# Optimization experiments

Hardware: AMD Instinct MI355X
Metric: run time of the kernel (lower is better)

## Reference

```python
import jax, jax.numpy as jnp
import numpy as np

NUM_GRAPHS = 256


def _mean_aggregate(h, src, dst, num_nodes):
    # DGL copy_src + mean reduce: dst node gets mean of src-node features over in-edges.
    summed = jax.ops.segment_sum(h[src], dst, num_segments=num_nodes)  # [N, F]
    deg = jax.ops.segment_sum(jnp.ones((src.shape[0],), h.dtype), dst, num_segments=num_nodes)
    return summed / jnp.maximum(deg, 1.0)[:, None]


def setup_inputs() -> dict:
    key = jax.random.key(0)
    ks = jax.random.split(key, 10)
    N, E, D_IN, H1, H2, OUT = 50000, 800000, 128, 256, 128, 1
    s = lambda fan: 1.0 / np.sqrt(fan)
    return {
        "h": jax.random.normal(ks[0], (N, D_IN), jnp.float32),
        "src": jax.random.randint(ks[1], (E,), 0, N),
        "dst": jax.random.randint(ks[2], (E,), 0, N),
        "graph_ids": jnp.sort(jax.random.randint(ks[3], (N,), 0, NUM_GRAPHS)),
        "W1": jax.random.normal(ks[4], (D_IN, H1), jnp.float32) * s(D_IN),
        "b1": jnp.zeros((H1,), jnp.float32),
        "W2": jax.random.normal(ks[5], (H1, H1), jnp.float32) * s(H1),
        "b2": jnp.zeros((H1,), jnp.float32),
        "Wr1": jax.random.normal(ks[6], (H1, H2), jnp.float32) * s(H1),
        "br1": jnp.zeros((H2,), jnp.float32),
        "Wr2": jax.random.normal(ks[7], (H2, OUT), jnp.float32) * s(H2),
        "br2": jnp.zeros((OUT,), jnp.float32),
    }


def reference(h, src, dst, graph_ids, W1, b1, W2, b2, Wr1, br1, Wr2, br2):
    N = h.shape[0]
    # GCN layer 1: mean-aggregate then linear+ReLU
    h = _mean_aggregate(h, src, dst, N)
    h = jax.nn.relu(h @ W1 + b1)
    # GCN layer 2
    h = _mean_aggregate(h, src, dst, N)
    h = jax.nn.relu(h @ W2 + b2)
    # dgl.mean_nodes readout: per-graph mean of node features
    gsum = jax.ops.segment_sum(h, graph_ids, num_segments=NUM_GRAPHS)  # [G, H1]
    gcnt = jax.ops.segment_sum(jnp.ones((N,), h.dtype), graph_ids, num_segments=NUM_GRAPHS)
    hg = gsum / jnp.maximum(gcnt, 1.0)[:, None]
    hidden = hg @ Wr1 + br1
    return hidden @ Wr2 + br2  # [G, 1]
```

## Files before the change

### kernel.cpp

```cpp
#include <hip/hip_runtime.h>


#define NUM_GRAPHS 256

#define CNT_B0 0
#define CNT_NB 1024
#define CST_B0 (CNT_B0 + CNT_NB)
#define CST_NB 512
#define GST_B0 (CST_B0 + CST_NB)
#define GST_NB 64
#define WT1_B0 (GST_B0 + GST_NB)
#define WT1_NB 16
#define WT2_B0 (WT1_B0 + WT1_NB)
#define WT2_NB 32
#define MISC_NB (WT2_B0 + WT2_NB)

typedef __attribute__((ext_vector_type(8))) short bf16x8;
typedef __attribute__((ext_vector_type(4))) float f32x4;

__device__ inline unsigned short f2bf(float f) {
    unsigned u = __float_as_uint(f);
    return (unsigned short)((u + 0x7fff + ((u >> 16) & 1)) >> 16);
}
__device__ inline float bflo(unsigned u) { return __uint_as_float(u << 16); }
__device__ inline float bfhi(unsigned u) { return __uint_as_float(u & 0xffff0000u); }


__launch_bounds__(256)
__global__ void misc_kernel(const int* __restrict__ dst, const int* __restrict__ gids,
                            const float* __restrict__ h,
                            const float* __restrict__ W1, const float* __restrict__ W2,
                            int* __restrict__ cnt, int* __restrict__ gstart,
                            unsigned short* __restrict__ hb,
                            unsigned short* __restrict__ Wt1, unsigned short* __restrict__ Wt2,
                            int N, int E) {
    int b = blockIdx.x, tid = threadIdx.x;
    if (b < CST_B0) {
        int lid = (b - CNT_B0) * 256 + tid;
        for (int e = lid; e < E; e += CNT_NB * 256) atomicAdd(&cnt[dst[e]], 1);
    } else if (b < GST_B0) {
        int lid = (b - CST_B0) * 256 + tid;
        int total4 = N * 32;
        for (int i = lid; i < total4; i += CST_NB * 256) {
            float4 v = *(const float4*)(h + (size_t)i * 4);
            ushort4 o;
            o.x = f2bf(v.x); o.y = f2bf(v.y); o.z = f2bf(v.z); o.w = f2bf(v.w);
            *(ushort4*)(hb + (size_t)i * 4) = o;
        }
    } else if (b < WT1_B0) {
        int lid = (b - GST_B0) * 256 + tid;
        for (int n = lid; n < N; n += GST_NB * 256) {
            int g = gids[n];
            int gp = (n == 0) ? -1 : gids[n - 1];
            for (int x = gp + 1; x <= g; ++x) gstart[x] = n;
            if (n == N - 1)
                for (int x = g + 1; x <= NUM_GRAPHS; ++x) gstart[x] = N;
        }
    } else if (b < WT2_B0) {
        int lid = (b - WT1_B0) * 256 + tid;
        for (int i = lid; i < 256 * 128; i += WT1_NB * 256)
            Wt1[i] = f2bf(W1[(size_t)(i & 127) * 256 + (i >> 7)]);
    } else {
        int lid = (b - WT2_B0) * 256 + tid;
        for (int i = lid; i < 256 * 256; i += WT2_NB * 256)
            Wt2[i] = f2bf(W2[(size_t)(i & 255) * 256 + (i >> 8)]);
    }
}


__global__ void scan1_kernel(const int* __restrict__ cnt, int* __restrict__ offs,
                             int* __restrict__ part, int N) {
    __shared__ int wsum[16];
    int tid = threadIdx.x;
    int lane = tid & 63;
    int wid = tid >> 6;
    int i = blockIdx.x * 1024 + tid;
    int v = (i < N) ? cnt[i] : 0;
    int x = v;
    #pragma unroll
    for (int d = 1; d < 64; d <<= 1) {
        int y = __shfl_up(x, d, 64);
        if (lane >= d) x += y;
    }
    if (lane == 63) wsum[wid] = x;
    __syncthreads();
    if (wid == 0) {
        int s = (lane < 16) ? wsum[lane] : 0;
        #pragma unroll
        for (int d = 1; d < 16; d <<= 1) {
            int y = __shfl_up(s, d, 64);
            if (lane >= d) s += y;
        }
        if (lane < 16) wsum[lane] = s;
    }
    __syncthreads();
    int wbase = (wid > 0) ? wsum[wid - 1] : 0;
    if (i < N) offs[i] = wbase + x - v;
    if (tid == 1023) part[blockIdx.x] = wbase + x;
}

__global__ void scan23_kernel(int* __restrict__ offs, const int* __restrict__ part,
                              int N, int E) {
    int b = blockIdx.x;
    int base = 0;
    for (int j = 0; j < b; ++j) base += part[j];
    int i = b * 1024 + threadIdx.x;
    if (i < N) offs[i] += base;
    if (b == 0 && threadIdx.x == 0) offs[N] = E;
}

__global__ void scatter_kernel(const int* __restrict__ src, const int* __restrict__ dst,
                               const int* __restrict__ offs, int* __restrict__ cnt,
                               int* __restrict__ eidx, int E) {
    int e = blockIdx.x * blockDim.x + threadIdx.x;
    if (e < E) {
        int d = dst[e];
        int p = offs[d] + atomicSub(&cnt[d], 1) - 1;
        eidx[p] = src[e];
    }
}


template <int D>
__global__ void agg_mean_bf16_kernel(const unsigned short* __restrict__ feat,
                                     const int* __restrict__ offs,
                                     const int* __restrict__ eidx,
                                     unsigned short* __restrict__ out, int N) {
    constexpr int VPL = D / 64;
    int wave = blockIdx.x * (blockDim.x >> 6) + (threadIdx.x >> 6);
    int lane = threadIdx.x & 63;
    if (wave >= N) return;
    int beg = offs[wave], end = offs[wave + 1];
    float acc[VPL];
    #pragma unroll
    for (int i = 0; i < VPL; ++i) acc[i] = 0.0f;

    int j = beg;
    for (; j + 8 <= end; j += 8) {
        int s[8];
        #pragma unroll
        for (int u = 0; u < 8; ++u) s[u] = eidx[j + u];
        if constexpr (VPL == 2) {
            unsigned v[8];
            #pragma unroll
            for (int u = 0; u < 8; ++u)
                v[u] = *(const unsigned*)(feat + (size_t)s[u] * D + lane * 2);
            #pragma unroll
            for (int u = 0; u < 8; ++u) { acc[0] += bflo(v[u]); acc[1] += bfhi(v[u]); }
        } else {
            uint2 v[8];
            #pragma unroll
            for (int u = 0; u < 8; ++u)
                v[u] = *(const uint2*)(feat + (size_t)s[u] * D + lane * 4);
            #pragma unroll
            for (int u = 0; u < 8; ++u) {
                acc[0] += bflo(v[u].x); acc[1] += bfhi(v[u].x);
                acc[2] += bflo(v[u].y); acc[3] += bfhi(v[u].y);
            }
        }
    }
    for (; j < end; ++j) {
        int s = eidx[j];
        if constexpr (VPL == 2) {
            unsigned v = *(const unsigned*)(feat + (size_t)s * D + lane * 2);
            acc[0] += bflo(v); acc[1] += bfhi(v);
        } else {
            uint2 v = *(const uint2*)(feat + (size_t)s * D + lane * 4);
            acc[0] += bflo(v.x); acc[1] += bfhi(v.x);
            acc[2] += bflo(v.y); acc[3] += bfhi(v.y);
        }
    }

    int deg = end - beg;
    float invd = 1.0f / (float)(deg > 0 ? deg : 1);
    unsigned short* orow = out + (size_t)wave * D + lane * VPL;
    if constexpr (VPL == 2) {
        ushort2 o; o.x = f2bf(acc[0] * invd); o.y = f2bf(acc[1] * invd);
        *(ushort2*)orow = o;
    } else {
        ushort4 o;
        o.x = f2bf(acc[0] * invd); o.y = f2bf(acc[1] * invd);
        o.z = f2bf(acc[2] * invd); o.w = f2bf(acc[3] * invd);
        *(ushort4*)orow = o;
    }
}


template <int K, int MODE>
__launch_bounds__(256)
__global__ void gemm_mfma_kernel(const unsigned short* __restrict__ A,
                                 const unsigned short* __restrict__ Wt,
                                 const float* __restrict__ bias,
                                 unsigned short* __restrict__ Cb,
                                 const int* __restrict__ gids,
                                 float* __restrict__ gsum,
                                 int N) {
    constexpr int LDS = 40;
    __shared__ unsigned short As[64 * LDS];
    __shared__ unsigned short Bs[256 * LDS];

    int tid = threadIdx.x;
    int wave = tid >> 6;
    int lane = tid & 63;
    int m = lane & 15;
    int q = lane >> 4;
    int rowBase = blockIdx.x * 64;

    f32x4 acc[4][4] = {};

    for (int kc = 0; kc < K; kc += 32) {
        {
            int r = tid >> 2;
            int seg = tid & 3;
            int gr = rowBase + r;
            uint4 v = make_uint4(0, 0, 0, 0);
            if (gr < N) v = *(const uint4*)(A + (size_t)gr * K + kc + seg * 8);
            *(uint4*)&As[r * LDS + seg * 8] = v;
        }
        #pragma unroll
        for (int it = 0; it < 4; ++it) {
            int n = (tid >> 2) + it * 64;
            int seg = tid & 3;
            uint4 v = *(const uint4*)(Wt + (size_t)n * K + kc + seg * 8);
            *(uint4*)&Bs[n * LDS + seg * 8] = v;
        }
        __syncthreads();

        bf16x8 af[4], bfr[4];
        #pragma unroll
        for (int r = 0; r < 4; ++r)
            af[r] = *(const bf16x8*)&As[(r * 16 + m) * LDS + q * 8];
        #pragma unroll
        for (int c = 0; c < 4; ++c)
            bfr[c] = *(const bf16x8*)&Bs[(wave * 64 + c * 16 + m) * LDS + q * 8];
        #pragma unroll
        for (int r = 0; r < 4; ++r)
            #pragma unroll
            for (int c = 0; c < 4; ++c)
                acc[r][c] = __builtin_amdgcn_mfma_f32_16x16x32_bf16(af[r], bfr[c], acc[r][c], 0, 0, 0);
        __syncthreads();
    }

    if constexpr (MODE == 0) {
        #pragma unroll
        for (int c = 0; c < 4; ++c) {
            int col = wave * 64 + c * 16 + m;
            float bv = bias[col];
            #pragma unroll
            for (int r = 0; r < 4; ++r) {
                #pragma unroll
                for (int reg = 0; reg < 4; ++reg) {
                    int grow = rowBase + r * 16 + q * 4 + reg;
                    if (grow < N)
                        Cb[(size_t)grow * 256 + col] = f2bf(fmaxf(acc[r][c][reg] + bv, 0.0f));
                }
            }
        }
    } else {
        int* sgid = (int*)As;
        if (tid < 64) {
            int gr = rowBase + tid;
            sgid[tid] = (gr < N) ? gids[gr] : -1;
        }
        __syncthreads();
        #pragma unroll
        for (int c = 0; c < 4; ++c) {
            int col = wave * 64 + c * 16 + m;
            float bv = bias[col];
            float partsum = 0.0f;
            int gprev = -1;
            #pragma unroll
            for (int r = 0; r < 4; ++r) {
                #pragma unroll
                for (int reg = 0; reg < 4; ++reg) {
                    int lr = r * 16 + q * 4 + reg;
                    if (rowBase + lr < N) {
                        int g = sgid[lr];
                        float o = fmaxf(acc[r][c][reg] + bv, 0.0f);
                        if (g != gprev) {
                            if (gprev >= 0) atomicAdd(&gsum[gprev * 256 + col], partsum);
                            partsum = 0.0f;
                            gprev = g;
                        }
                        partsum += o;
                    }
                }
            }
            if (gprev >= 0) atomicAdd(&gsum[gprev * 256 + col], partsum);
        }
    }
}


__global__ void final_kernel(const float* __restrict__ gsum, const int* __restrict__ gstart,
                             const float* __restrict__ Wr1, const float* __restrict__ br1,
                             const float* __restrict__ Wr2, const float* __restrict__ br2,
                             float* __restrict__ out) {
    int g = blockIdx.x;
    int j = threadIdx.x;
    int c = gstart[g + 1] - gstart[g];
    float invc = 1.0f / (float)(c > 0 ? c : 1);
    const float* gs = gsum + g * 256;
    float acc = br1[j];
    for (int k = 0; k < 256; ++k)
        acc += (gs[k] * invc) * Wr1[k * 128 + j];
    float p = acc * Wr2[j];
    #pragma unroll
    for (int d = 32; d > 0; d >>= 1) p += __shfl_down(p, d, 64);
    __shared__ float ws2[2];
    if ((j & 63) == 0) ws2[j >> 6] = p;
    __syncthreads();
    if (j == 0) out[g] = ws2[0] + ws2[1] + br2[0];
}


extern "C" void kernel_launch(void* const* d_in, const int* in_sizes, int n_in,
                              void* d_out, int out_size, void* d_ws, size_t ws_size,
                              hipStream_t stream) {
    const float* h    = (const float*)d_in[0];
    const int*   src  = (const int*)d_in[1];
    const int*   dst  = (const int*)d_in[2];
    const int*   gids = (const int*)d_in[3];
    const float* W1   = (const float*)d_in[4];
    const float* b1   = (const float*)d_in[5];
    const float* W2   = (const float*)d_in[6];
    const float* b2   = (const float*)d_in[7];
    const float* Wr1  = (const float*)d_in[8];
    const float* br1  = (const float*)d_in[9];
    const float* Wr2  = (const float*)d_in[10];
    const float* br2  = (const float*)d_in[11];

    int N = in_sizes[0] / 128;
    int E = in_sizes[1];
    int nScanBlocks = (N + 1023) / 1024;

    char* w = (char*)d_ws;
    unsigned short* hb     = (unsigned short*)w;  w += (size_t)N * 128 * sizeof(unsigned short);
    unsigned short* h1b    = (unsigned short*)w;  w += (size_t)N * 256 * sizeof(unsigned short);
    unsigned short* aggOut = (unsigned short*)w;  w += (size_t)N * 256 * sizeof(unsigned short);
    int* cnt    = (int*)w;              w += (size_t)N * sizeof(int);
    float* gsum = (float*)w;            w += (size_t)NUM_GRAPHS * 256 * sizeof(float);
    int* offs   = (int*)w;              w += (size_t)(N + 1) * sizeof(int);
    int* eidx   = (int*)w;              w += (size_t)E * sizeof(int);
    int* part   = (int*)w;              w += 64 * sizeof(int);
    unsigned short* Wt1 = (unsigned short*)w;  w += 256 * 128 * sizeof(unsigned short);
    unsigned short* Wt2 = (unsigned short*)w;  w += 256 * 256 * sizeof(unsigned short);
    int* gstart = (int*)w;              w += (size_t)(NUM_GRAPHS + 1) * sizeof(int);

    hipMemsetAsync(cnt, 0, (size_t)N * sizeof(int) + (size_t)NUM_GRAPHS * 256 * sizeof(float),
                   stream);
    misc_kernel<<<MISC_NB, 256, 0, stream>>>(dst, gids, h, W1, W2, cnt, gstart, hb, Wt1, Wt2, N, E);
    scan1_kernel<<<nScanBlocks, 1024, 0, stream>>>(cnt, offs, part, N);
    scan23_kernel<<<nScanBlocks, 1024, 0, stream>>>(offs, part, N, E);
    scatter_kernel<<<(E + 255) / 256, 256, 0, stream>>>(src, dst, offs, cnt, eidx, E);

    agg_mean_bf16_kernel<128><<<(N + 3) / 4, 256, 0, stream>>>(hb, offs, eidx, aggOut, N);
    gemm_mfma_kernel<128, 0><<<(N + 63) / 64, 256, 0, stream>>>(aggOut, Wt1, b1, h1b, nullptr, nullptr, N);

    agg_mean_bf16_kernel<256><<<(N + 3) / 4, 256, 0, stream>>>(h1b, offs, eidx, aggOut, N);
    gemm_mfma_kernel<256, 1><<<(N + 63) / 64, 256, 0, stream>>>(aggOut, Wt2, b2, nullptr, gids, gsum, N);

    final_kernel<<<NUM_GRAPHS, 128, 0, stream>>>(gsum, gstart, Wr1, br1, Wr2, br2, (float*)d_out);
}
```

Baseline: 346.9 us.

## Fuse mean aggregation into MFMA GEMM and precompute edge ranks for CSR scatter

```diff
diff --git a/kernel.cpp b/kernel.cpp
--- a/kernel.cpp
+++ b/kernel.cpp
@@ -30,14 +30,19 @@
 __global__ void misc_kernel(const int* __restrict__ dst, const int* __restrict__ gids,
                             const float* __restrict__ h,
                             const float* __restrict__ W1, const float* __restrict__ W2,
-                            int* __restrict__ cnt, int* __restrict__ gstart,
+                            int* __restrict__ cnt, int* __restrict__ rank,
+                            int* __restrict__ gstart,
                             unsigned short* __restrict__ hb,
                             unsigned short* __restrict__ Wt1, unsigned short* __restrict__ Wt2,
                             int N, int E) {
     int b = blockIdx.x, tid = threadIdx.x;
     if (b < CST_B0) {
         int lid = (b - CNT_B0) * 256 + tid;
-        for (int e = lid; e < E; e += CNT_NB * 256) atomicAdd(&cnt[dst[e]], 1);
+        for (int e = lid; e < E; e += CNT_NB * 256) {
+            int d = __builtin_nontemporal_load(&dst[e]);
+            int r = atomicAdd(&cnt[d], 1);
+            __builtin_nontemporal_store(r, &rank[e]);
+        }
     } else if (b < GST_B0) {
         int lid = (b - CST_B0) * 256 + tid;
         int total4 = N * 32;
@@ -109,132 +114,127 @@
     if (b == 0 && threadIdx.x == 0) offs[N] = E;
 }
 
+
 __global__ void scatter_kernel(const int* __restrict__ src, const int* __restrict__ dst,
-                               const int* __restrict__ offs, int* __restrict__ cnt,
+                               const int* __restrict__ offs, const int* __restrict__ rank,
                                int* __restrict__ eidx, int E) {
     int e = blockIdx.x * blockDim.x + threadIdx.x;
     if (e < E) {
-        int d = dst[e];
-        int p = offs[d] + atomicSub(&cnt[d], 1) - 1;
-        eidx[p] = src[e];
-    }
-}
-
-
-template <int D>
-__global__ void agg_mean_bf16_kernel(const unsigned short* __restrict__ feat,
-                                     const int* __restrict__ offs,
-                                     const int* __restrict__ eidx,
-                                     unsigned short* __restrict__ out, int N) {
-    constexpr int VPL = D / 64;
-    int wave = blockIdx.x * (blockDim.x >> 6) + (threadIdx.x >> 6);
-    int lane = threadIdx.x & 63;
-    if (wave >= N) return;
-    int beg = offs[wave], end = offs[wave + 1];
-    float acc[VPL];
-    #pragma unroll
-    for (int i = 0; i < VPL; ++i) acc[i] = 0.0f;
-
-    int j = beg;
-    for (; j + 8 <= end; j += 8) {
-        int s[8];
-        #pragma unroll
-        for (int u = 0; u < 8; ++u) s[u] = eidx[j + u];
-        if constexpr (VPL == 2) {
-            unsigned v[8];
-            #pragma unroll
-            for (int u = 0; u < 8; ++u)
-                v[u] = *(const unsigned*)(feat + (size_t)s[u] * D + lane * 2);
-            #pragma unroll
-            for (int u = 0; u < 8; ++u) { acc[0] += bflo(v[u]); acc[1] += bfhi(v[u]); }
-        } else {
-            uint2 v[8];
-            #pragma unroll
-            for (int u = 0; u < 8; ++u)
-                v[u] = *(const uint2*)(feat + (size_t)s[u] * D + lane * 4);
-            #pragma unroll
-            for (int u = 0; u < 8; ++u) {
-                acc[0] += bflo(v[u].x); acc[1] += bfhi(v[u].x);
-                acc[2] += bflo(v[u].y); acc[3] += bfhi(v[u].y);
-            }
-        }
-    }
-    for (; j < end; ++j) {
-        int s = eidx[j];
-        if constexpr (VPL == 2) {
-            unsigned v = *(const unsigned*)(feat + (size_t)s * D + lane * 2);
-            acc[0] += bflo(v); acc[1] += bfhi(v);
-        } else {
-            uint2 v = *(const uint2*)(feat + (size_t)s * D + lane * 4);
-            acc[0] += bflo(v.x); acc[1] += bfhi(v.x);
-            acc[2] += bflo(v.y); acc[3] += bfhi(v.y);
-        }
-    }
-
-    int deg = end - beg;
-    float invd = 1.0f / (float)(deg > 0 ? deg : 1);
-    unsigned short* orow = out + (size_t)wave * D + lane * VPL;
-    if constexpr (VPL == 2) {
-        ushort2 o; o.x = f2bf(acc[0] * invd); o.y = f2bf(acc[1] * invd);
-        *(ushort2*)orow = o;
-    } else {
-        ushort4 o;
-        o.x = f2bf(acc[0] * invd); o.y = f2bf(acc[1] * invd);
-        o.z = f2bf(acc[2] * invd); o.w = f2bf(acc[3] * invd);
-        *(ushort4*)orow = o;
+        int d = __builtin_nontemporal_load(&dst[e]);
+        int r = __builtin_nontemporal_load(&rank[e]);
+        int s = __builtin_nontemporal_load(&src[e]);
+        eidx[offs[d] + r] = s;
     }
 }
 
 
 template <int K, int MODE>
 __launch_bounds__(256)
-__global__ void gemm_mfma_kernel(const unsigned short* __restrict__ A,
-                                 const unsigned short* __restrict__ Wt,
-                                 const float* __restrict__ bias,
-                                 unsigned short* __restrict__ Cb,
-                                 const int* __restrict__ gids,
-                                 float* __restrict__ gsum,
-                                 int N) {
-    constexpr int LDS = 40;
-    __shared__ unsigned short As[64 * LDS];
-    __shared__ unsigned short Bs[256 * LDS];
+__global__ void gemm_agg_kernel(const unsigned short* __restrict__ feat,
+                                const int* __restrict__ offs,
+                                const int* __restrict__ eidx,
+                                const unsigned short* __restrict__ Wt,
+                                const float* __restrict__ bias,
+                                unsigned short* __restrict__ Cb,
+                                const int* __restrict__ gids,
+                                float* __restrict__ gsum,
+                                int N) {
+    constexpr int LDSA = K + 8;
+    constexpr int LDSB = 40;
+    __shared__ unsigned short As[32 * LDSA];
+    __shared__ unsigned short Bs[256 * LDSB];
 
     int tid = threadIdx.x;
     int wave = tid >> 6;
     int lane = tid & 63;
     int m = lane & 15;
     int q = lane >> 4;
-    int rowBase = blockIdx.x * 64;
-
-    f32x4 acc[4][4] = {};
-
+    int rowBase = blockIdx.x * 32;
+
+    for (int t = 0; t < 8; ++t) {
+        int r = wave * 8 + t;
+        int n = rowBase + r;
+        if constexpr (K == 128) {
+            float a0 = 0.0f, a1 = 0.0f;
+            if (n < N) {
+                int beg = offs[n], end = offs[n + 1];
+                int j = beg;
+                for (; j + 8 <= end; j += 8) {
+                    int s[8];
+                    #pragma unroll
+                    for (int u = 0; u < 8; ++u) s[u] = eidx[j + u];
+                    unsigned v[8];
+                    #pragma unroll
+                    for (int u = 0; u < 8; ++u)
+                        v[u] = *(const unsigned*)(feat + (size_t)s[u] * 128 + lane * 2);
+                    #pragma unroll
+                    for (int u = 0; u < 8; ++u) { a0 += bflo(v[u]); a1 += bfhi(v[u]); }
+                }
+                for (; j < end; ++j) {
+                    unsigned v = *(const unsigned*)(feat + (size_t)eidx[j] * 128 + lane * 2);
+                    a0 += bflo(v); a1 += bfhi(v);
+                }
+                int deg = end - beg;
+                float invd = 1.0f / (float)(deg > 0 ? deg : 1);
+                a0 *= invd; a1 *= invd;
+            }
+            ushort2 o; o.x = f2bf(a0); o.y = f2bf(a1);
+            *(ushort2*)&As[r * LDSA + lane * 2] = o;
+        } else {
+            float a0 = 0.0f, a1 = 0.0f, a2 = 0.0f, a3 = 0.0f;
+            if (n < N) {
+                int beg = offs[n], end = offs[n + 1];
+                int j = beg;
+                for (; j + 8 <= end; j += 8) {
+                    int s[8];
+                    #pragma unroll
+                    for (int u = 0; u < 8; ++u) s[u] = eidx[j + u];
+                    uint2 v[8];
+                    #pragma unroll
+                    for (int u = 0; u < 8; ++u)
+                        v[u] = *(const uint2*)(feat + (size_t)s[u] * 256 + lane * 4);
+                    #pragma unroll
+                    for (int u = 0; u < 8; ++u) {
+                        a0 += bflo(v[u].x); a1 += bfhi(v[u].x);
+                        a2 += bflo(v[u].y); a3 += bfhi(v[u].y);
+                    }
+                }
+                for (; j < end; ++j) {
+                    uint2 v = *(const uint2*)(feat + (size_t)eidx[j] * 256 + lane * 4);
+                    a0 += bflo(v.x); a1 += bfhi(v.x);
+                    a2 += bflo(v.y); a3 += bfhi(v.y);
+                }
+                int deg = end - beg;
+                float invd = 1.0f / (float)(deg > 0 ? deg : 1);
+                a0 *= invd; a1 *= invd; a2 *= invd; a3 *= invd;
+            }
+            ushort4 o;
+            o.x = f2bf(a0); o.y = f2bf(a1); o.z = f2bf(a2); o.w = f2bf(a3);
+            *(ushort4*)&As[r * LDSA + lane * 4] = o;
+        }
+    }
+    __syncthreads();
+
+    f32x4 acc[2][4] = {};
     for (int kc = 0; kc < K; kc += 32) {
-        {
-            int r = tid >> 2;
-            int seg = tid & 3;
-            int gr = rowBase + r;
-            uint4 v = make_uint4(0, 0, 0, 0);
-            if (gr < N) v = *(const uint4*)(A + (size_t)gr * K + kc + seg * 8);
-            *(uint4*)&As[r * LDS + seg * 8] = v;
-        }
         #pragma unroll
         for (int it = 0; it < 4; ++it) {
             int n = (tid >> 2) + it * 64;
             int seg = tid & 3;
             uint4 v = *(const uint4*)(Wt + (size_t)n * K + kc + seg * 8);
-            *(uint4*)&Bs[n * LDS + seg * 8] = v;
+            *(uint4*)&Bs[n * LDSB + seg * 8] = v;
         }
         __syncthreads();
 
-        bf16x8 af[4], bfr[4];
-        #pragma unroll
-        for (int r = 0; r < 4; ++r)
-            af[r] = *(const bf16x8*)&As[(r * 16 + m) * LDS + q * 8];
+        bf16x8 af[2], bfr[4];
+        #pragma unroll
+        for (int r = 0; r < 2; ++r)
+            af[r] = *(const bf16x8*)&As[(r * 16 + m) * LDSA + kc + q * 8];
         #pragma unroll
         for (int c = 0; c < 4; ++c)
-            bfr[c] = *(const bf16x8*)&Bs[(wave * 64 + c * 16 + m) * LDS + q * 8];
-        #pragma unroll
-        for (int r = 0; r < 4; ++r)
+            bfr[c] = *(const bf16x8*)&Bs[(wave * 64 + c * 16 + m) * LDSB + q * 8];
+        #pragma unroll
+        for (int r = 0; r < 2; ++r)
             #pragma unroll
             for (int c = 0; c < 4; ++c)
                 acc[r][c] = __builtin_amdgcn_mfma_f32_16x16x32_bf16(af[r], bfr[c], acc[r][c], 0, 0, 0);
@@ -247,7 +247,7 @@
             int col = wave * 64 + c * 16 + m;
             float bv = bias[col];
             #pragma unroll
-            for (int r = 0; r < 4; ++r) {
+            for (int r = 0; r < 2; ++r) {
                 #pragma unroll
                 for (int reg = 0; reg < 4; ++reg) {
                     int grow = rowBase + r * 16 + q * 4 + reg;
@@ -257,8 +257,8 @@
             }
         }
     } else {
-        int* sgid = (int*)As;
-        if (tid < 64) {
+        int* sgid = (int*)Bs;
+        if (tid < 32) {
             int gr = rowBase + tid;
             sgid[tid] = (gr < N) ? gids[gr] : -1;
         }
@@ -270,7 +270,7 @@
             float partsum = 0.0f;
             int gprev = -1;
             #pragma unroll
-            for (int r = 0; r < 4; ++r) {
+            for (int r = 0; r < 2; ++r) {
                 #pragma unroll
                 for (int reg = 0; reg < 4; ++reg) {
                     int lr = r * 16 + q * 4 + reg;
@@ -335,13 +335,13 @@
     int nScanBlocks = (N + 1023) / 1024;
 
     char* w = (char*)d_ws;
-    unsigned short* hb     = (unsigned short*)w;  w += (size_t)N * 128 * sizeof(unsigned short);
-    unsigned short* h1b    = (unsigned short*)w;  w += (size_t)N * 256 * sizeof(unsigned short);
-    unsigned short* aggOut = (unsigned short*)w;  w += (size_t)N * 256 * sizeof(unsigned short);
+    unsigned short* hb  = (unsigned short*)w;  w += (size_t)N * 128 * sizeof(unsigned short);
+    unsigned short* h1b = (unsigned short*)w;  w += (size_t)N * 256 * sizeof(unsigned short);
     int* cnt    = (int*)w;              w += (size_t)N * sizeof(int);
     float* gsum = (float*)w;            w += (size_t)NUM_GRAPHS * 256 * sizeof(float);
     int* offs   = (int*)w;              w += (size_t)(N + 1) * sizeof(int);
     int* eidx   = (int*)w;              w += (size_t)E * sizeof(int);
+    int* rank   = (int*)w;              w += (size_t)E * sizeof(int);
     int* part   = (int*)w;              w += 64 * sizeof(int);
     unsigned short* Wt1 = (unsigned short*)w;  w += 256 * 128 * sizeof(unsigned short);
     unsigned short* Wt2 = (unsigned short*)w;  w += 256 * 256 * sizeof(unsigned short);
@@ -349,16 +349,15 @@
 
     hipMemsetAsync(cnt, 0, (size_t)N * sizeof(int) + (size_t)NUM_GRAPHS * 256 * sizeof(float),
                    stream);
-    misc_kernel<<<MISC_NB, 256, 0, stream>>>(dst, gids, h, W1, W2, cnt, gstart, hb, Wt1, Wt2, N, E);
+    misc_kernel<<<MISC_NB, 256, 0, stream>>>(dst, gids, h, W1, W2, cnt, rank, gstart,
+                                             hb, Wt1, Wt2, N, E);
     scan1_kernel<<<nScanBlocks, 1024, 0, stream>>>(cnt, offs, part, N);
     scan23_kernel<<<nScanBlocks, 1024, 0, stream>>>(offs, part, N, E);
-    scatter_kernel<<<(E + 255) / 256, 256, 0, stream>>>(src, dst, offs, cnt, eidx, E);
-
-    agg_mean_bf16_kernel<128><<<(N + 3) / 4, 256, 0, stream>>>(hb, offs, eidx, aggOut, N);
-    gemm_mfma_kernel<128, 0><<<(N + 63) / 64, 256, 0, stream>>>(aggOut, Wt1, b1, h1b, nullptr, nullptr, N);
-
-    agg_mean_bf16_kernel<256><<<(N + 3) / 4, 256, 0, stream>>>(h1b, offs, eidx, aggOut, N);
-    gemm_mfma_kernel<256, 1><<<(N + 63) / 64, 256, 0, stream>>>(aggOut, Wt2, b2, nullptr, gids, gsum, N);
-
+    scatter_kernel<<<(E + 255) / 256, 256, 0, stream>>>(src, dst, offs, rank, eidx, E);
+
+    gemm_agg_kernel<128, 0><<<(N + 31) / 32, 256, 0, stream>>>(hb, offs, eidx, Wt1, b1,
+                                                               h1b, nullptr, nullptr, N);
+    gemm_agg_kernel<256, 1><<<(N + 31) / 32, 256, 0, stream>>>(h1b, offs, eidx, Wt2, b2,
+                                                               nullptr, gids, gsum, N);
     final_kernel<<<NUM_GRAPHS, 128, 0, stream>>>(gsum, gstart, Wr1, br1, Wr2, br2, (float*)d_out);
 }
```

Result: no change. 352.2 us (+1.5%).
